# Optimization experiments

Hardware: AMD Instinct MI355X
Metric: run time of the kernel (lower is better)

The kernel has to match this reference:

```python
import jax, jax.numpy as jnp
import numpy as np

N = 1_000_000
W = 20  # layer_width


def setup_inputs() -> dict:
    key = jax.random.key(0)
    ks = jax.random.split(key, 8)
    s = 0.5  # modest init scale for tanh net
    return {
        "t": jax.random.normal(ks[0], (N, 1), dtype=jnp.float32),
        "W1": jax.random.normal(ks[1], (1, W), dtype=jnp.float32) * s,
        "b1": jnp.zeros((W,), jnp.float32),
        "W2": jax.random.normal(ks[2], (W, W), dtype=jnp.float32) * s / np.sqrt(W),
        "b2": jnp.zeros((W,), jnp.float32),
        "W3": jax.random.normal(ks[3], (W, W), dtype=jnp.float32) * s / np.sqrt(W),
        "b3": jnp.zeros((W,), jnp.float32),
        "W4": jax.random.normal(ks[4], (W, W), dtype=jnp.float32) * s / np.sqrt(W),
        "b4": jnp.zeros((W,), jnp.float32),
        "Wo": jax.random.normal(ks[5], (W, 3), dtype=jnp.float32) * s / np.sqrt(W),
        "bo": jnp.zeros((3,), jnp.float32),
        "c1": jnp.float32(1.0),
        "c2": jnpp if False else jnp.float32(1.0),
        "c3": jnp.float32(1.0),
    }


def reference(t, W1, b1, W2, b2, W3, b3, W4, b4, Wo, bo, c1, c2, c3):
    # DenseBlock(4, 20): four tanh hidden layers + linear head to [x, y, z]
    def mlp(tt):
        h = jnp.tanh(tt @ W1 + b1)
        h = jnp.tanh(h @ W2 + b2)
        h = jnp.tanh(h @ W3 + b3)
        h = jnp.tanh(h @ W4 + b4)
        return h @ Wo + bo  # [N, 3]

    # forward-mode AD: one JVP pass gives d[x,y,z]/dt for every sample
    out, dout = jax.jvp(mlp, (t,), (jnp.ones_like(t),))
    x, y, z = out[:, 0:1], out[:, 1:2], out[:, 2:3]
    dx, dy, dz = dout[:, 0:1], dout[:, 1:2], dout[:, 2:3]
    # Lorenz residuals (log_opt=False -> vars used directly)
    fx = dx - c1 * (y - x)
    fy = dy - x * (c2 - z) + y
    fz = dz - x * y + c3 * z
    return jnp.concatenate([x, y, z, fx, fy, fz], axis=1)  # [N, 6]
```

## Files before the change

kernel.cpp:

```cpp
#include <hip/hip_runtime.h>

#define NBLK 256

__device__ __forceinline__ float fast_tanh(float x) {
    float e = __builtin_amdgcn_exp2f(x * 2.88539008f);
    return 1.0f - 2.0f * __builtin_amdgcn_rcpf(e + 1.0f);
}

__global__ __launch_bounds__(NBLK) void pinn_kernel(
    const float* __restrict__ T,
    const float* __restrict__ W1, const float* __restrict__ b1,
    const float* __restrict__ W2, const float* __restrict__ b2,
    const float* __restrict__ W3, const float* __restrict__ b3,
    const float* __restrict__ W4, const float* __restrict__ b4,
    const float* __restrict__ Wo, const float* __restrict__ bo,
    const float* __restrict__ C1, const float* __restrict__ C2, const float* __restrict__ C3,
    float* __restrict__ out, int n)
{
    const int i0 = blockIdx.x * NBLK + threadIdx.x;
    const int i  = (i0 < n) ? i0 : (n - 1);
    const float t = T[i];

    float h[20], d[20];

#pragma unroll
    for (int j = 0; j < 20; ++j) {
        const float w = W1[j];
        const float e = fast_tanh(fmaf(t, w, b1[j]));
        h[j] = e;
        d[j] = (1.0f - e * e) * w;
    }

#pragma unroll 1
    for (int L = 0; L < 3; ++L) {
        const float* __restrict__ WP = (L == 0) ? W2 : (L == 1) ? W3 : W4;
        const float* __restrict__ BP = (L == 0) ? b2 : (L == 1) ? b3 : b4;
        float a[20], dd[20];
#pragma unroll
        for (int j = 0; j < 20; ++j) { a[j] = BP[j]; dd[j] = 0.0f; }
#pragma unroll
        for (int k = 0; k < 20; ++k) {
            const float hk = h[k], dk = d[k];
#pragma unroll
            for (int j = 0; j < 20; ++j) {
                const float w = WP[k * 20 + j];
                a[j]  = fmaf(hk, w, a[j]);
                dd[j] = fmaf(dk, w, dd[j]);
            }
        }
#pragma unroll
        for (int j = 0; j < 20; ++j) {
            const float e = fast_tanh(a[j]);
            h[j] = e;
            d[j] = (1.0f - e * e) * dd[j];
        }
    }

    float o0 = bo[0], o1 = bo[1], o2 = bo[2];
    float g0 = 0.0f, g1 = 0.0f, g2 = 0.0f;
#pragma unroll
    for (int k = 0; k < 20; ++k) {
        const float hk = h[k], dk = d[k];
        const float w0 = Wo[k * 3 + 0];
        const float w1 = Wo[k * 3 + 1];
        const float w2 = Wo[k * 3 + 2];
        o0 = fmaf(hk, w0, o0);  g0 = fmaf(dk, w0, g0);
        o1 = fmaf(hk, w1, o1);  g1 = fmaf(dk, w1, g1);
        o2 = fmaf(hk, w2, o2);  g2 = fmaf(dk, w2, g2);
    }

    const float x = o0, y = o1, zz = o2;
    const float c1 = C1[0], c2 = C2[0], c3 = C3[0];
    const float fx = g0 - c1 * (y - x);
    const float fy = g1 - x * (c2 - zz) + y;
    const float fz = g2 - x * y + c3 * zz;

    if (i0 < n) {
        float2* po = reinterpret_cast<float2*>(out + (size_t)i0 * 6);
        po[0] = make_float2(x,  y);
        po[1] = make_float2(zz, fx);
        po[2] = make_float2(fy, fz);
    }
}

extern "C" void kernel_launch(void* const* d_in, const int* in_sizes, int n_in,
                              void* d_out, int out_size, void* d_ws, size_t ws_size,
                              hipStream_t stream) {
    const float* T  = (const float*)d_in[0];
    const float* W1 = (const float*)d_in[1];
    const float* b1 = (const float*)d_in[2];
    const float* W2 = (const float*)d_in[3];
    const float* b2 = (const float*)d_in[4];
    const float* W3 = (const float*)d_in[5];
    const float* b3 = (const float*)d_in[6];
    const float* W4 = (const float*)d_in[7];
    const float* b4 = (const float*)d_in[8];
    const float* Wo = (const float*)d_in[9];
    const float* bo = (const float*)d_in[10];
    const float* C1 = (const float*)d_in[11];
    const float* C2 = (const float*)d_in[12];
    const float* C3 = (const float*)d_in[13];
    float* out = (float*)d_out;

    const int n = in_sizes[0];
    const int blocks = (n + NBLK - 1) / NBLK;
    pinn_kernel<<<blocks, NBLK, 0, stream>>>(T, W1, b1, W2, b2, W3, b3, W4, b4,
                                             Wo, bo, C1, C2, C3, out, n);
}
```

Baseline: 162.9 us.

## Vectorize MLP JVP with packed FP32 FMAs and vector weight loads

Rewrites the per-sample MLP forward and tangent pass to use two-wide float vectors so the compiler can emit packed FP32 FMA instructions (v_pk_fma_f32), roughly halving the FMA instruction count. Weights are loaded as float4 vectors, and an opaque zero offset forces them into vector registers instead of scalar loads. The three hidden layers are fully unrolled via a macro instead of a runtime loop. The output head is split into paired partial sums that are reduced at the end. This raises register pressure and replaces broadcast scalar weight loads with per-lane vector loads, which may reduce occupancy or add memory traffic.

```diff
diff --git a/kernel.cpp b/kernel.cpp
--- a/kernel.cpp
+++ b/kernel.cpp
@@ -2,9 +2,24 @@
 
 #define NBLK 256
 
-__device__ __forceinline__ float fast_tanh(float x) {
-    float e = __builtin_amdgcn_exp2f(x * 2.88539008f);
-    return 1.0f - 2.0f * __builtin_amdgcn_rcpf(e + 1.0f);
+typedef float f2 __attribute__((ext_vector_type(2)));
+typedef float f4 __attribute__((ext_vector_type(4)));
+
+static __device__ __forceinline__ f2 pk_fma(f2 a, f2 b, f2 c) {
+#if __has_builtin(__builtin_elementwise_fma)
+    return __builtin_elementwise_fma(a, b, c);
+#else
+    f2 r; r.x = fmaf(a.x, b.x, c.x); r.y = fmaf(a.y, b.y, c.y); return r;
+#endif
+}
+
+__device__ __forceinline__ void tanh2(const f2 z, f2& th, f2& om) {
+    const f2 zz = z * 2.88539008f;
+    f2 s;
+    s.x = __builtin_amdgcn_rcpf(__builtin_amdgcn_exp2f(zz.x) + 1.0f);
+    s.y = __builtin_amdgcn_rcpf(__builtin_amdgcn_exp2f(zz.y) + 1.0f);
+    th = 1.0f - 2.0f * s;
+    om = 1.0f - th * th;
 }
 
 __global__ __launch_bounds__(NBLK) void pinn_kernel(
@@ -21,59 +36,104 @@
     const int i  = (i0 < n) ? i0 : (n - 1);
     const float t = T[i];
 
-    float h[20], d[20];
+    int vz = 0;
+    asm volatile("" : "+v"(vz));
 
+    f2 H[10], D[10];
+    const f2 t2 = {t, t};
+
+    {
+        const f4* __restrict__ W1v = reinterpret_cast<const f4*>(W1);
+        const f4* __restrict__ b1v = reinterpret_cast<const f4*>(b1);
 #pragma unroll
-    for (int j = 0; j < 20; ++j) {
-        const float w = W1[j];
-        const float e = fast_tanh(fmaf(t, w, b1[j]));
-        h[j] = e;
-        d[j] = (1.0f - e * e) * w;
-    }
-
-#pragma unroll 1
-    for (int L = 0; L < 3; ++L) {
-        const float* __restrict__ WP = (L == 0) ? W2 : (L == 1) ? W3 : W4;
-        const float* __restrict__ BP = (L == 0) ? b2 : (L == 1) ? b3 : b4;
-        float a[20], dd[20];
-#pragma unroll
-        for (int j = 0; j < 20; ++j) { a[j] = BP[j]; dd[j] = 0.0f; }
-#pragma unroll
-        for (int k = 0; k < 20; ++k) {
-            const float hk = h[k], dk = d[k];
-#pragma unroll
-            for (int j = 0; j < 20; ++j) {
-                const float w = WP[k * 20 + j];
-                a[j]  = fmaf(hk, w, a[j]);
-                dd[j] = fmaf(dk, w, dd[j]);
-            }
-        }
-#pragma unroll
-        for (int j = 0; j < 20; ++j) {
-            const float e = fast_tanh(a[j]);
-            h[j] = e;
-            d[j] = (1.0f - e * e) * dd[j];
+        for (int q = 0; q < 5; ++q) {
+            const f4 w4 = W1v[vz + q];
+            const f4 b4 = b1v[vz + q];
+            const f2 wa = {w4.x, w4.y}, wb = {w4.z, w4.w};
+            const f2 ba = {b4.x, b4.y}, bb = {b4.z, b4.w};
+            f2 th, om;
+            tanh2(pk_fma(t2, wa, ba), th, om);
+            H[2*q]   = th;  D[2*q]   = om * wa;
+            tanh2(pk_fma(t2, wb, bb), th, om);
+            H[2*q+1] = th;  D[2*q+1] = om * wb;
         }
     }
 
-    float o0 = bo[0], o1 = bo[1], o2 = bo[2];
-    float g0 = 0.0f, g1 = 0.0f, g2 = 0.0f;
+#define LAYER(WP, BP) do {                                                      \
+        const f4* __restrict__ Wv = reinterpret_cast<const f4*>(WP);            \
+        const f4* __restrict__ Bv = reinterpret_cast<const f4*>(BP);            \
+        f2 A[10], DD[10];                                                       \
+        _Pragma("unroll")                                                       \
+        for (int q = 0; q < 5; ++q) {                                           \
+            const f4 b4 = Bv[vz + q];                                           \
+            A[2*q]    = (f2){b4.x, b4.y};                                       \
+            A[2*q+1]  = (f2){b4.z, b4.w};                                       \
+            DD[2*q]   = (f2){0.0f, 0.0f};                                       \
+            DD[2*q+1] = (f2){0.0f, 0.0f};                                       \
+        }                                                                       \
+        _Pragma("unroll")                                                       \
+        for (int k = 0; k < 20; ++k) {                                          \
+            const float hk = (k & 1) ? H[k >> 1].y : H[k >> 1].x;               \
+            const float dk = (k & 1) ? D[k >> 1].y : D[k >> 1].x;               \
+            const f2 hk2 = {hk, hk};                                            \
+            const f2 dk2 = {dk, dk};                                            \
+            _Pragma("unroll")                                                   \
+            for (int q = 0; q < 5; ++q) {                                       \
+                const f4 w4 = Wv[vz + k*5 + q];                                 \
+                const f2 wa = {w4.x, w4.y}, wb = {w4.z, w4.w};                  \
+                A[2*q]    = pk_fma(hk2, wa, A[2*q]);                            \
+                A[2*q+1]  = pk_fma(hk2, wb, A[2*q+1]);                          \
+                DD[2*q]   = pk_fma(dk2, wa, DD[2*q]);                           \
+                DD[2*q+1] = pk_fma(dk2, wb, DD[2*q+1]);                         \
+            }                                                                   \
+        }                                                                       \
+        _Pragma("unroll")                                                       \
+        for (int jj = 0; jj < 10; ++jj) {                                       \
+            f2 th, om;                                                          \
+            tanh2(A[jj], th, om);                                               \
+            H[jj] = th;                                                         \
+            D[jj] = om * DD[jj];                                                \
+        }                                                                       \
+    } while (0)
+
+    LAYER(W2, b2);
+    LAYER(W3, b3);
+    LAYER(W4, b4);
+#undef LAYER
+
+    f4 WoR[15];
+    {
+        const f4* __restrict__ Wov = reinterpret_cast<const f4*>(Wo);
 #pragma unroll
-    for (int k = 0; k < 20; ++k) {
-        const float hk = h[k], dk = d[k];
-        const float w0 = Wo[k * 3 + 0];
-        const float w1 = Wo[k * 3 + 1];
-        const float w2 = Wo[k * 3 + 2];
-        o0 = fmaf(hk, w0, o0);  g0 = fmaf(dk, w0, g0);
-        o1 = fmaf(hk, w1, o1);  g1 = fmaf(dk, w1, g1);
-        o2 = fmaf(hk, w2, o2);  g2 = fmaf(dk, w2, g2);
+        for (int m = 0; m < 15; ++m) WoR[m] = Wov[vz + m];
     }
+#define WOF(k, j) (((3*(k)+(j)) & 3) == 0 ? WoR[(3*(k)+(j)) >> 2].x : \
+                   ((3*(k)+(j)) & 3) == 1 ? WoR[(3*(k)+(j)) >> 2].y : \
+                   ((3*(k)+(j)) & 3) == 2 ? WoR[(3*(k)+(j)) >> 2].z : \
+                                            WoR[(3*(k)+(j)) >> 2].w)
+    f2 o0 = {0,0}, o1 = {0,0}, o2 = {0,0}, g0 = {0,0}, g1 = {0,0}, g2 = {0,0};
+#pragma unroll
+    for (int kk = 0; kk < 10; ++kk) {
+        const f2 hp = H[kk], dp = D[kk];
+        const f2 w0 = { WOF(2*kk, 0), WOF(2*kk+1, 0) };
+        const f2 w1 = { WOF(2*kk, 1), WOF(2*kk+1, 1) };
+        const f2 w2 = { WOF(2*kk, 2), WOF(2*kk+1, 2) };
+        o0 = pk_fma(hp, w0, o0);  g0 = pk_fma(dp, w0, g0);
+        o1 = pk_fma(hp, w1, o1);  g1 = pk_fma(dp, w1, g1);
+        o2 = pk_fma(hp, w2, o2);  g2 = pk_fma(dp, w2, g2);
+    }
+#undef WOF
 
-    const float x = o0, y = o1, zz = o2;
+    const float x   = o0.x + o0.y + bo[0];
+    const float y   = o1.x + o1.y + bo[1];
+    const float zz  = o2.x + o2.y + bo[2];
+    const float dx  = g0.x + g0.y;
+    const float dy  = g1.x + g1.y;
+    const float dz  = g2.x + g2.y;
     const float c1 = C1[0], c2 = C2[0], c3 = C3[0];
-    const float fx = g0 - c1 * (y - x);
-    const float fy = g1 - x * (c2 - zz) + y;
-    const float fz = g2 - x * y + c3 * zz;
+    const float fx = dx - c1 * (y - x);
+    const float fy = dy - x * (c2 - zz) + y;
+    const float fz = dz - x * y + c3 * zz;
 
     if (i0 < n) {
         float2* po = reinterpret_cast<float2*>(out + (size_t)i0 * 6);
```

Result: slower. 239.6 us (+47.1%).
